# Kernel tuning notes

Hardware: AMD Instinct MI355X
Metric: run time of the kernel (lower is better)

The kernel has to match this reference:

```python
import jax, jax.numpy as jnp
import numpy as np

MAX_STEPS = 128  # upper bound on ACT halting steps (forces halt at last step)
EPS = 0.01


def setup_inputs() -> dict:
    key = jax.random.key(0)
    ks = jax.random.split(key, 8)
    IN, H, OUT = 4096, 4096, 4096
    def lin(k, fan_in, shape):
        return jax.random.normal(k, shape, jnp.float32) / np.float32(np.sqrt(fan_in))
    return {
        "x": jax.random.normal(ks[0], (IN,), jnp.float32),
        "s": jax.random.normal(ks[1], (H,), jnp.float32),
        "W_hidden": lin(ks[2], 1 + IN + H, (H, 1 + IN + H)),
        "b_hidden": lin(ks[3], 1 + IN + H, (H,)),
        "W_halt": lin(ks[4], H, (1, H)),
        "b_halt": lin(ks[5], H, (1,)),
        "W_out": lin(ks[6], H, (OUT, H)),
        "b_out": lin(ks[7], H, (OUT,)),
    }


def _act_forward(x, s, W_hidden, b_hidden, W_halt, b_halt, W_out, b_out):
    OUT = W_out.shape[0]

    def step(carry, i):
        state, cum, acc_out, acc_state, done, ponder = carry
        # flag = 1 on the first step (x1), 0 afterwards (x0)
        flag = jnp.where(i == 0, 1.0, 0.0).astype(x.dtype)
        z = jnp.concatenate([flag[None], x, state])          # [1+IN+H]
        new_state = W_hidden @ z + b_hidden                  # [H]
        p = jax.nn.sigmoid(W_halt @ new_state + b_halt)[0]   # scalar halt prob
        will_halt = (cum + p >= 1.0 - EPS) | (i == MAX_STEPS - 1)
        active = jnp.logical_not(done)
        # last step's weight is the remainder 1 - sum(previous p)
        w = jnp.where(active, jnp.where(will_halt, 1.0 - cum, p), 0.0)
        acc_out = acc_out + w * (W_out @ new_state + b_out)
        acc_state = acc_state + w * new_state
        ponder = jnp.where(active & will_halt,
                           i.astype(x.dtype) + 1.0 + (1.0 - cum), ponder)
        state = jnp.where(active, new_state, state)
        cum = jnp.where(active, cum + p, cum)
        done = done | will_halt
        return (state, cum, acc_out, acc_state, done, ponder), None

    init = (s,
            jnp.zeros((), x.dtype),
            jnp.zeros((OUT,), x.dtype),
            jnp.zeros_like(s),
            jnp.zeros((), jnp.bool_),
            jnp.zeros((), x.dtype))
    (state, cum, out, hid, done, ponder), _ = jax.lax.scan(
        step, init, jnp.arange(MAX_STEPS))
    return out, hid, ponder[None]


def reference(x, s, W_hidden, b_hidden, W_halt, b_halt, W_out, b_out):
    return _act_forward(x, s, W_hidden, b_hidden, W_halt, b_halt, W_out, b_out)
```

## Files before the change

### kernel.cpp

```cpp
#include <hip/hip_runtime.h>
#include <hip/hip_cooperative_groups.h>

namespace cg = cooperative_groups;

#define K_PRE 6

#define O_CUM    0
#define O_DONE   128
#define O_WSUM   256
#define O_PONDER 257
#define O_AXB    512
#define O_P0     4608
#define O_Q0     12800
#define O_ACCH   20992
#define O_NS0    25088
#define O_NS1    29184

__device__ __forceinline__ int zi(int c) { return c + (c >> 5); }

__global__ __launch_bounds__(1024) void k_step(
    int i,
    const float* __restrict__ x, const float* __restrict__ s,
    const float* __restrict__ Wh, const float* __restrict__ bh,
    const float* __restrict__ Whalt, const float* __restrict__ bhalt,
    float* __restrict__ wsb)
{
    const int tid  = threadIdx.x;
    const int lane = tid & 63;
    const int wid  = tid >> 6;
    const int q    = blockIdx.x >> 8;
    const int row  = ((blockIdx.x & 255) << 4) + wid;

    __shared__ float zb[4225];
    __shared__ float red[16];

    const int pre = (4 - ((row + 1) & 3)) & 3;
    float* pbW = wsb + ((i & 1) ? O_Q0 : O_P0);

    if (i == 0) {
        const float* src = q ? s : x;
        for (int k = tid; k < 4096; k += 1024) zb[zi(k)] = src[k];
        __syncthreads();

        const float* WhR = Wh + (size_t)row * 8193;
        const int start  = q ? 4097 : 1;
        const int n4     = (4096 - pre) >> 2;
        const float4* W4 = reinterpret_cast<const float4*>(WhR + start + pre);
        float a0=0.f, a1=0.f, a2=0.f, a3=0.f;
        if (lane < pre) a0 = WhR[start + lane] * zb[zi(lane)];
        #pragma unroll 8
        for (int j = lane; j < n4; j += 64) {
            float4 wv = W4[j];
            int c = pre + 4 * j;
            a0 += wv.x * zb[zi(c)];
            a1 += wv.y * zb[zi(c + 1)];
            a2 += wv.z * zb[zi(c + 2)];
            a3 += wv.w * zb[zi(c + 3)];
        }
        for (int c = pre + 4 * n4 + lane; c < 4096; c += 64)
            a0 += WhR[start + c] * zb[zi(c)];
        float acc = (a0 + a1) + (a2 + a3);
        #pragma unroll
        for (int off = 32; off; off >>= 1) acc += __shfl_xor(acc, off, 64);
        if (lane == 0) {
            if (q == 0) {
                wsb[O_AXB + row] = acc + bh[row];
                pbW[row]         = acc + WhR[0];
            } else {
                pbW[4096 + row]  = acc;
            }
        }
        return;
    }

    const float doneB = (i >= 2) ? wsb[O_DONE + i - 2] : 0.0f;
    if (doneB != 0.0f) {
        if (blockIdx.x == 0 && tid == 0) {
            wsb[O_CUM + i - 1]  = wsb[O_CUM + i - 2];
            wsb[O_DONE + i - 1] = 1.0f;
        }
        return;
    }
    const float cumB = (i >= 2) ? wsb[O_CUM + i - 2] : 0.0f;

    const float* pbR  = wsb + (((i - 1) & 1) ? O_Q0 : O_P0);
    const float* bias = (i == 1) ? bh : (wsb + O_AXB);
    float4 u0 = reinterpret_cast<const float4*>(pbR)[tid];
    float4 u1 = reinterpret_cast<const float4*>(pbR + 4096)[tid];
    float4 bb = reinterpret_cast<const float4*>(bias)[tid];
    float4 hw = reinterpret_cast<const float4*>(Whalt)[tid];
    float4 nsv;
    nsv.x = u0.x + u1.x + bb.x;  nsv.y = u0.y + u1.y + bb.y;
    nsv.z = u0.z + u1.z + bb.z;  nsv.w = u0.w + u1.w + bb.w;
    if ((tid >> 9) == q) {
        int lc = 4 * tid - 2048 * q;
        zb[zi(lc)]   = nsv.x; zb[zi(lc+1)] = nsv.y;
        zb[zi(lc+2)] = nsv.z; zb[zi(lc+3)] = nsv.w;
    }
    float part = hw.x*nsv.x + hw.y*nsv.y + hw.z*nsv.z + hw.w*nsv.w;
    #pragma unroll
    for (int off = 32; off; off >>= 1) part += __shfl_xor(part, off, 64);
    if (lane == 0) red[wid] = part;
    __syncthreads();
    float logit = bhalt[0];
    #pragma unroll
    for (int j = 0; j < 16; ++j) logit += red[j];
    const float p         = 1.0f / (1.0f + expf(-logit));
    const bool  will_halt = (cumB + p >= 0.99f) || ((i - 1) == 127);
    const float w         = will_halt ? (1.0f - cumB) : p;

    if (blockIdx.x == 0 && tid == 0) {
        wsb[O_CUM + i - 1]  = cumB + p;
        wsb[O_DONE + i - 1] = will_halt ? 1.0f : 0.0f;
        if (i == 1) wsb[O_WSUM] = w; else wsb[O_WSUM] += w;
        if (will_halt) wsb[O_PONDER] = (float)(i - 1) + 1.0f + (1.0f - cumB);
    }
    if (blockIdx.x == 0) {
        float4* aH = reinterpret_cast<float4*>(wsb + O_ACCH);
        if (i == 1) {
            float4 t; t.x = w*nsv.x; t.y = w*nsv.y; t.z = w*nsv.z; t.w = w*nsv.w;
            aH[tid] = t;
        } else {
            float4 t = aH[tid];
            t.x += w*nsv.x; t.y += w*nsv.y; t.z += w*nsv.z; t.w += w*nsv.w;
            aH[tid] = t;
        }
    }
    if (i == K_PRE && blockIdx.x == 1)
        reinterpret_cast<float4*>(wsb + (((i - 1) & 1) ? O_NS1 : O_NS0))[tid] = nsv;

    if (i < K_PRE && !will_halt) {
        const float* WhR = Wh + (size_t)row * 8193;
        const int start  = 4097 + 2048 * q;
        const int n4     = (2048 - pre) >> 2;
        const float4* W4 = reinterpret_cast<const float4*>(WhR + start + pre);
        float a0=0.f, a1=0.f, a2=0.f, a3=0.f;
        if (lane < pre) a0 = WhR[start + lane] * zb[zi(lane)];
        #pragma unroll 8
        for (int j = lane; j < n4; j += 64) {
            float4 wv = W4[j];
            int c = pre + 4 * j;
            a0 += wv.x * zb[zi(c)];
            a1 += wv.y * zb[zi(c + 1)];
            a2 += wv.z * zb[zi(c + 2)];
            a3 += wv.w * zb[zi(c + 3)];
        }
        for (int c = pre + 4 * n4 + lane; c < 2048; c += 64)
            a0 += WhR[start + c] * zb[zi(c)];
        float acc = (a0 + a1) + (a2 + a3);
        #pragma unroll
        for (int off = 32; off; off >>= 1) acc += __shfl_xor(acc, off, 64);
        if (lane == 0) pbW[(q << 12) + row] = acc;
    }
}

__global__ __launch_bounds__(1024, 4) void k_tail(
    const float* __restrict__ x, const float* __restrict__ Wh,
    const float* __restrict__ bh, const float* __restrict__ Whalt,
    const float* __restrict__ bhalt, float* __restrict__ wsb)
{
    cg::grid_group grid = cg::this_grid();
    if (wsb[O_DONE + K_PRE - 1] != 0.0f) return;

    const int tid  = threadIdx.x;
    const int lane = tid & 63;
    const int wid  = tid >> 6;
    const int gw   = blockIdx.x * 16 + wid;

    float* ns0 = wsb + O_NS0;
    float* ns1 = wsb + O_NS1;

    __shared__ float xl[4096];
    __shared__ float red[16];
    for (int k = tid; k < 4096; k += 1024) xl[k] = x[k];
    __syncthreads();

    const float* WhR   = Wh + (size_t)gw * 8193;
    const float4* wh4  = reinterpret_cast<const float4*>(Whalt);
    const float bh_r   = bh[gw];
    const float bhalt0 = bhalt[0];

    float cum = wsb[O_CUM + K_PRE - 1];
    float wsuml = 0.f, ponder = 0.f;

    for (int i = K_PRE; i < 128; ++i) {
        const float* st = (i & 1) ? ns0 : ns1;
        float*      nsc = (i & 1) ? ns1 : ns0;

        float acc = 0.0f;
        #pragma unroll 8
        for (int k = lane; k < 4096; k += 64) acc += WhR[1 + k] * xl[k];
        #pragma unroll 8
        for (int k = lane; k < 4096; k += 64) acc += WhR[4097 + k] * st[k];
        #pragma unroll
        for (int off = 32; off; off >>= 1) acc += __shfl_xor(acc, off, 64);
        if (lane == 0) nsc[gw] = acc + bh_r;
        grid.sync();

        const float4* ns4 = reinterpret_cast<const float4*>(nsc);
        float4 nv = ns4[tid], hw = wh4[tid];
        float part = hw.x*nv.x + hw.y*nv.y + hw.z*nv.z + hw.w*nv.w;
        #pragma unroll
        for (int off = 32; off; off >>= 1) part += __shfl_xor(part, off, 64);
        if (lane == 0) red[wid] = part;
        __syncthreads();
        float logit = bhalt0;
        #pragma unroll
        for (int j = 0; j < 16; ++j) logit += red[j];
        const float p         = 1.0f / (1.0f + expf(-logit));
        const bool  will_halt = (cum + p >= 0.99f) || (i == 127);
        const float w         = will_halt ? (1.0f - cum) : p;

        if (blockIdx.x == 0) {
            float4* aH = reinterpret_cast<float4*>(wsb + O_ACCH);
            float4 t = aH[tid];
            t.x += w*nv.x; t.y += w*nv.y; t.z += w*nv.z; t.w += w*nv.w;
            aH[tid] = t;
        }
        wsuml += w;

        if (will_halt) { ponder = (float)i + 1.0f + (1.0f - cum); break; }
        cum += p;
        grid.sync();
    }

    if (blockIdx.x == 0 && tid == 0) {
        wsb[O_WSUM]  += wsuml;
        wsb[O_PONDER] = ponder;
    }
}

__global__ __launch_bounds__(1024) void k_out(
    const float* __restrict__ Wo, const float* __restrict__ bo,
    const float* __restrict__ wsb, float* __restrict__ out)
{
    const int tid  = threadIdx.x;
    const int lane = tid & 63;
    const int wid  = tid >> 6;
    const int row  = blockIdx.x * 16 + wid;

    __shared__ float zb[4225];
    for (int k = tid; k < 4096; k += 1024) zb[zi(k)] = wsb[O_ACCH + k];
    __syncthreads();

    const float4* Wo4 = reinterpret_cast<const float4*>(Wo + (size_t)row * 4096);
    float b0=0.f, b1=0.f, b2=0.f, b3=0.f;
    #pragma unroll 8
    for (int j = lane; j < 1024; j += 64) {
        float4 wv = Wo4[j];
        int c = 4 * j;
        b0 += wv.x * zb[zi(c)];
        b1 += wv.y * zb[zi(c + 1)];
        b2 += wv.z * zb[zi(c + 2)];
        b3 += wv.w * zb[zi(c + 3)];
    }
    float acc = (b0 + b1) + (b2 + b3);
    #pragma unroll
    for (int off = 32; off; off >>= 1) acc += __shfl_xor(acc, off, 64);
    if (lane == 0) out[row] = acc + wsb[O_WSUM] * bo[row];

    const int gtid = blockIdx.x * 1024 + tid;
    if (gtid < 4096) out[4096 + gtid] = wsb[O_ACCH + gtid];
    if (gtid == 0)   out[8192] = wsb[O_PONDER];
}

extern "C" void kernel_launch(void* const* d_in, const int* in_sizes, int n_in,
                              void* d_out, int out_size, void* d_ws, size_t ws_size,
                              hipStream_t stream) {
    const float* x     = (const float*)d_in[0];
    const float* s     = (const float*)d_in[1];
    const float* Wh    = (const float*)d_in[2];
    const float* bh    = (const float*)d_in[3];
    const float* Whalt = (const float*)d_in[4];
    const float* bhalt = (const float*)d_in[5];
    const float* Wo    = (const float*)d_in[6];
    const float* bo    = (const float*)d_in[7];
    float* out = (float*)d_out;
    float* wsb = (float*)d_ws;

    for (int i = 0; i <= K_PRE; ++i)
        k_step<<<512, 1024, 0, stream>>>(i, x, s, Wh, bh, Whalt, bhalt, wsb);

    {
        void* args[] = { (void*)&x, (void*)&Wh, (void*)&bh, (void*)&Whalt,
                         (void*)&bhalt, (void*)&wsb };
        hipLaunchCooperativeKernel((void*)k_tail, dim3(256), dim3(1024),
                                   args, 0, stream);
    }
    k_out<<<256, 1024, 0, stream>>>(Wo, bo, wsb, out);
}
```

Before: 193.2 us.

## Stage weight rows into LDS via async global_load_lds and halve k_step grid

```diff
diff --git a/kernel.cpp b/kernel.cpp
--- a/kernel.cpp
+++ b/kernel.cpp
@@ -18,6 +18,21 @@
 
 __device__ __forceinline__ int zi(int c) { return c + (c >> 5); }
 
+__device__ __forceinline__ void stage512(const float4* __restrict__ g, int nf4,
+                                         float4* wb, int lane) {
+    #pragma unroll
+    for (int k = 0; k < 8; ++k) {
+        int jj = (k << 6) + lane;
+        if (jj >= nf4) jj = nf4 - 1;
+        __builtin_amdgcn_global_load_lds(
+            (const __attribute__((address_space(1))) void*)(g + jj),
+            (__attribute__((address_space(3))) void*)(wb + (k << 6)), 16, 0, 0);
+    }
+}
+
+#define WAIT_VM0   asm volatile("s_waitcnt vmcnt(0)" ::: "memory")
+#define WAIT_LGKM0 asm volatile("s_waitcnt lgkmcnt(0)" ::: "memory")
+
 __global__ __launch_bounds__(1024) void k_step(
     int i,
     const float* __restrict__ x, const float* __restrict__ s,
@@ -28,47 +43,84 @@
     const int tid  = threadIdx.x;
     const int lane = tid & 63;
     const int wid  = tid >> 6;
-    const int q    = blockIdx.x >> 8;
-    const int row  = ((blockIdx.x & 255) << 4) + wid;
-
-    __shared__ float zb[4225];
-    __shared__ float red[16];
+    const int row  = blockIdx.x * 16 + wid;
+
+    __shared__ float  zb[4225];
+    __shared__ float  red[16];
+    __shared__ float4 wbuf[16][512];
+    float4* wb = wbuf[wid];
 
     const int pre = (4 - ((row + 1) & 3)) & 3;
     float* pbW = wsb + ((i & 1) ? O_Q0 : O_P0);
+    const float* WhR = Wh + (size_t)row * 8193;
 
     if (i == 0) {
-        const float* src = q ? s : x;
-        for (int k = tid; k < 4096; k += 1024) zb[zi(k)] = src[k];
+        for (int k = tid; k < 4096; k += 1024) zb[zi(k)] = x[k];
         __syncthreads();
-
-        const float* WhR = Wh + (size_t)row * 8193;
-        const int start  = q ? 4097 : 1;
-        const int n4     = (4096 - pre) >> 2;
-        const float4* W4 = reinterpret_cast<const float4*>(WhR + start + pre);
-        float a0=0.f, a1=0.f, a2=0.f, a3=0.f;
-        if (lane < pre) a0 = WhR[start + lane] * zb[zi(lane)];
-        #pragma unroll 8
-        for (int j = lane; j < n4; j += 64) {
-            float4 wv = W4[j];
-            int c = pre + 4 * j;
-            a0 += wv.x * zb[zi(c)];
-            a1 += wv.y * zb[zi(c + 1)];
-            a2 += wv.z * zb[zi(c + 2)];
-            a3 += wv.w * zb[zi(c + 3)];
-        }
-        for (int c = pre + 4 * n4 + lane; c < 4096; c += 64)
-            a0 += WhR[start + c] * zb[zi(c)];
-        float acc = (a0 + a1) + (a2 + a3);
-        #pragma unroll
-        for (int off = 32; off; off >>= 1) acc += __shfl_xor(acc, off, 64);
-        if (lane == 0) {
-            if (q == 0) {
+        {
+            const int start = 1, cs = start + pre, n4h = (4096 - pre) >> 2;
+            const float4* g = reinterpret_cast<const float4*>(WhR + cs);
+            stage512(g, 512, wb, lane);
+            float a0=0.f, a1=0.f, a2=0.f, a3=0.f;
+            if (lane < pre) a0 = WhR[start + lane] * zb[zi(lane)];
+            WAIT_VM0;
+            #pragma unroll 8
+            for (int j = lane; j < 512; j += 64) {
+                float4 wv = wb[j]; int c = pre + 4 * j;
+                a0 += wv.x * zb[zi(c)];   a1 += wv.y * zb[zi(c + 1)];
+                a2 += wv.z * zb[zi(c + 2)]; a3 += wv.w * zb[zi(c + 3)];
+            }
+            WAIT_LGKM0;
+            stage512(g + 512, n4h - 512, wb, lane);
+            WAIT_VM0;
+            #pragma unroll 8
+            for (int j = 512 + lane; j < n4h; j += 64) {
+                float4 wv = wb[j - 512]; int c = pre + 4 * j;
+                a0 += wv.x * zb[zi(c)];   a1 += wv.y * zb[zi(c + 1)];
+                a2 += wv.z * zb[zi(c + 2)]; a3 += wv.w * zb[zi(c + 3)];
+            }
+            for (int c = pre + 4 * n4h + lane; c < 4096; c += 64)
+                a0 += WhR[start + c] * zb[zi(c)];
+            float acc = (a0 + a1) + (a2 + a3);
+            #pragma unroll
+            for (int off = 32; off; off >>= 1) acc += __shfl_xor(acc, off, 64);
+            if (lane == 0) {
                 wsb[O_AXB + row] = acc + bh[row];
                 pbW[row]         = acc + WhR[0];
-            } else {
-                pbW[4096 + row]  = acc;
-            }
+            }
+        }
+        __syncthreads();
+        for (int k = tid; k < 4096; k += 1024) zb[zi(k)] = s[k];
+        __syncthreads();
+        {
+            const int start = 4097, cs = start + pre, n4h = (4096 - pre) >> 2;
+            const float4* g = reinterpret_cast<const float4*>(WhR + cs);
+            WAIT_LGKM0;
+            stage512(g, 512, wb, lane);
+            float a0=0.f, a1=0.f, a2=0.f, a3=0.f;
+            if (lane < pre) a0 = WhR[start + lane] * zb[zi(lane)];
+            WAIT_VM0;
+            #pragma unroll 8
+            for (int j = lane; j < 512; j += 64) {
+                float4 wv = wb[j]; int c = pre + 4 * j;
+                a0 += wv.x * zb[zi(c)];   a1 += wv.y * zb[zi(c + 1)];
+                a2 += wv.z * zb[zi(c + 2)]; a3 += wv.w * zb[zi(c + 3)];
+            }
+            WAIT_LGKM0;
+            stage512(g + 512, n4h - 512, wb, lane);
+            WAIT_VM0;
+            #pragma unroll 8
+            for (int j = 512 + lane; j < n4h; j += 64) {
+                float4 wv = wb[j - 512]; int c = pre + 4 * j;
+                a0 += wv.x * zb[zi(c)];   a1 += wv.y * zb[zi(c + 1)];
+                a2 += wv.z * zb[zi(c + 2)]; a3 += wv.w * zb[zi(c + 3)];
+            }
+            for (int c = pre + 4 * n4h + lane; c < 4096; c += 64)
+                a0 += WhR[start + c] * zb[zi(c)];
+            float acc = (a0 + a1) + (a2 + a3);
+            #pragma unroll
+            for (int off = 32; off; off >>= 1) acc += __shfl_xor(acc, off, 64);
+            if (lane == 0) pbW[4096 + row] = acc;
         }
         return;
     }
@@ -92,11 +144,9 @@
     float4 nsv;
     nsv.x = u0.x + u1.x + bb.x;  nsv.y = u0.y + u1.y + bb.y;
     nsv.z = u0.z + u1.z + bb.z;  nsv.w = u0.w + u1.w + bb.w;
-    if ((tid >> 9) == q) {
-        int lc = 4 * tid - 2048 * q;
-        zb[zi(lc)]   = nsv.x; zb[zi(lc+1)] = nsv.y;
-        zb[zi(lc+2)] = nsv.z; zb[zi(lc+3)] = nsv.w;
-    }
+    { int c = 4 * tid;
+      zb[zi(c)]   = nsv.x; zb[zi(c+1)] = nsv.y;
+      zb[zi(c+2)] = nsv.z; zb[zi(c+3)] = nsv.w; }
     float part = hw.x*nsv.x + hw.y*nsv.y + hw.z*nsv.z + hw.w*nsv.w;
     #pragma unroll
     for (int off = 32; off; off >>= 1) part += __shfl_xor(part, off, 64);
@@ -130,27 +180,31 @@
         reinterpret_cast<float4*>(wsb + (((i - 1) & 1) ? O_NS1 : O_NS0))[tid] = nsv;
 
     if (i < K_PRE && !will_halt) {
-        const float* WhR = Wh + (size_t)row * 8193;
-        const int start  = 4097 + 2048 * q;
-        const int n4     = (2048 - pre) >> 2;
-        const float4* W4 = reinterpret_cast<const float4*>(WhR + start + pre);
-        float a0=0.f, a1=0.f, a2=0.f, a3=0.f;
-        if (lane < pre) a0 = WhR[start + lane] * zb[zi(lane)];
-        #pragma unroll 8
-        for (int j = lane; j < n4; j += 64) {
-            float4 wv = W4[j];
-            int c = pre + 4 * j;
-            a0 += wv.x * zb[zi(c)];
-            a1 += wv.y * zb[zi(c + 1)];
-            a2 += wv.z * zb[zi(c + 2)];
-            a3 += wv.w * zb[zi(c + 3)];
-        }
-        for (int c = pre + 4 * n4 + lane; c < 2048; c += 64)
-            a0 += WhR[start + c] * zb[zi(c)];
-        float acc = (a0 + a1) + (a2 + a3);
         #pragma unroll
-        for (int off = 32; off; off >>= 1) acc += __shfl_xor(acc, off, 64);
-        if (lane == 0) pbW[(q << 12) + row] = acc;
+        for (int q = 0; q < 2; ++q) {
+            const int startq = 4097 + 2048 * q;
+            const int csq    = startq + pre;
+            const int n4q    = (2048 - pre) >> 2;
+            const int zo     = 2048 * q;
+            const float4* gq = reinterpret_cast<const float4*>(WhR + csq);
+            WAIT_LGKM0;
+            stage512(gq, n4q, wb, lane);
+            float a0=0.f, a1=0.f, a2=0.f, a3=0.f;
+            if (lane < pre) a0 = WhR[startq + lane] * zb[zi(zo + lane)];
+            WAIT_VM0;
+            #pragma unroll 8
+            for (int j = lane; j < n4q; j += 64) {
+                float4 wv = wb[j]; int c = zo + pre + 4 * j;
+                a0 += wv.x * zb[zi(c)];   a1 += wv.y * zb[zi(c + 1)];
+                a2 += wv.z * zb[zi(c + 2)]; a3 += wv.w * zb[zi(c + 3)];
+            }
+            for (int c2 = pre + 4 * n4q + lane; c2 < 2048; c2 += 64)
+                a0 += WhR[startq + c2] * zb[zi(zo + c2)];
+            float acc = (a0 + a1) + (a2 + a3);
+            #pragma unroll
+            for (int off = 32; off; off >>= 1) acc += __shfl_xor(acc, off, 64);
+            if (lane == 0) pbW[(q << 12) + row] = acc;
+        }
     }
 }
 
@@ -239,20 +293,31 @@
     const int wid  = tid >> 6;
     const int row  = blockIdx.x * 16 + wid;
 
-    __shared__ float zb[4225];
+    __shared__ float  zb[4225];
+    __shared__ float4 wbuf[16][512];
+    float4* wb = wbuf[wid];
+
     for (int k = tid; k < 4096; k += 1024) zb[zi(k)] = wsb[O_ACCH + k];
     __syncthreads();
 
-    const float4* Wo4 = reinterpret_cast<const float4*>(Wo + (size_t)row * 4096);
+    const float4* WoR4 = reinterpret_cast<const float4*>(Wo + (size_t)row * 4096);
+    stage512(WoR4, 512, wb, lane);
     float b0=0.f, b1=0.f, b2=0.f, b3=0.f;
+    WAIT_VM0;
     #pragma unroll 8
-    for (int j = lane; j < 1024; j += 64) {
-        float4 wv = Wo4[j];
-        int c = 4 * j;
-        b0 += wv.x * zb[zi(c)];
-        b1 += wv.y * zb[zi(c + 1)];
-        b2 += wv.z * zb[zi(c + 2)];
-        b3 += wv.w * zb[zi(c + 3)];
+    for (int j = lane; j < 512; j += 64) {
+        float4 wv = wb[j]; int c = 4 * j;
+        b0 += wv.x * zb[zi(c)];   b1 += wv.y * zb[zi(c + 1)];
+        b2 += wv.z * zb[zi(c + 2)]; b3 += wv.w * zb[zi(c + 3)];
+    }
+    WAIT_LGKM0;
+    stage512(WoR4 + 512, 512, wb, lane);
+    WAIT_VM0;
+    #pragma unroll 8
+    for (int j = 512 + lane; j < 1024; j += 64) {
+        float4 wv = wb[j - 512]; int c = 4 * j;
+        b0 += wv.x * zb[zi(c)];   b1 += wv.y * zb[zi(c + 1)];
+        b2 += wv.z * zb[zi(c + 2)]; b3 += wv.w * zb[zi(c + 3)];
     }
     float acc = (b0 + b1) + (b2 + b3);
     #pragma unroll
@@ -279,7 +344,7 @@
     float* wsb = (float*)d_ws;
 
     for (int i = 0; i <= K_PRE; ++i)
-        k_step<<<512, 1024, 0, stream>>>(i, x, s, Wh, bh, Whalt, bhalt, wsb);
+        k_step<<<256, 1024, 0, stream>>>(i, x, s, Wh, bh, Whalt, bhalt, wsb);
 
     {
         void* args[] = { (void*)&x, (void*)&Wh, (void*)&bh, (void*)&Whalt,
```

New measurement: 193.7 us. Within noise of the previous version (+0.2%).

## Restructure GEMV kernels to block-wide rows with batched float4 loads

Applied to the files above, without the earlier changes.

```diff
diff --git a/kernel.cpp b/kernel.cpp
--- a/kernel.cpp
+++ b/kernel.cpp
@@ -4,6 +4,8 @@
 namespace cg = cooperative_groups;
 
 #define K_PRE 6
+#define NB 256
+#define NT 1024
 
 #define O_CUM    0
 #define O_DONE   128
@@ -18,7 +20,7 @@
 
 __device__ __forceinline__ int zi(int c) { return c + (c >> 5); }
 
-__global__ __launch_bounds__(1024) void k_step(
+__global__ __launch_bounds__(NT) void k_step(
     int i,
     const float* __restrict__ x, const float* __restrict__ s,
     const float* __restrict__ Wh, const float* __restrict__ bh,
@@ -28,47 +30,72 @@
     const int tid  = threadIdx.x;
     const int lane = tid & 63;
     const int wid  = tid >> 6;
-    const int q    = blockIdx.x >> 8;
-    const int row  = ((blockIdx.x & 255) << 4) + wid;
-
-    __shared__ float zb[4225];
-    __shared__ float red[16];
-
-    const int pre = (4 - ((row + 1) & 3)) & 3;
+
+    __shared__ float zb1[4225];
+    __shared__ float zb2[4225];
+    __shared__ float redH[16];
+    __shared__ float redR[16][16];
+
     float* pbW = wsb + ((i & 1) ? O_Q0 : O_P0);
 
     if (i == 0) {
-        const float* src = q ? s : x;
-        for (int k = tid; k < 4096; k += 1024) zb[zi(k)] = src[k];
+        for (int k = tid; k < 4096; k += NT) { zb1[zi(k)] = x[k]; zb2[zi(k)] = s[k]; }
         __syncthreads();
-
-        const float* WhR = Wh + (size_t)row * 8193;
-        const int start  = q ? 4097 : 1;
-        const int n4     = (4096 - pre) >> 2;
-        const float4* W4 = reinterpret_cast<const float4*>(WhR + start + pre);
-        float a0=0.f, a1=0.f, a2=0.f, a3=0.f;
-        if (lane < pre) a0 = WhR[start + lane] * zb[zi(lane)];
-        #pragma unroll 8
-        for (int j = lane; j < n4; j += 64) {
-            float4 wv = W4[j];
-            int c = pre + 4 * j;
-            a0 += wv.x * zb[zi(c)];
-            a1 += wv.y * zb[zi(c + 1)];
-            a2 += wv.z * zb[zi(c + 2)];
-            a3 += wv.w * zb[zi(c + 3)];
-        }
-        for (int c = pre + 4 * n4 + lane; c < 4096; c += 64)
-            a0 += WhR[start + c] * zb[zi(c)];
-        float acc = (a0 + a1) + (a2 + a3);
-        #pragma unroll
-        for (int off = 32; off; off >>= 1) acc += __shfl_xor(acc, off, 64);
-        if (lane == 0) {
-            if (q == 0) {
-                wsb[O_AXB + row] = acc + bh[row];
-                pbW[row]         = acc + WhR[0];
-            } else {
-                pbW[4096 + row]  = acc;
-            }
+        for (int g = 0; g < 4; ++g) {
+            float4 wx[4], wsv[4];
+            float  px[4], ps[4];
+            int    pres[4], n4s[4];
+            #pragma unroll
+            for (int rr = 0; rr < 4; ++rr) {
+                const int row = blockIdx.x * 16 + g * 4 + rr;
+                const int pre = (4 - ((row + 1) & 3)) & 3;
+                const int n4  = (4096 - pre) >> 2;
+                pres[rr] = pre; n4s[rr] = n4;
+                const float* base = Wh + (size_t)row * 8193;
+                if (tid < n4) {
+                    wx[rr]  = *(const float4*)(base + 1    + pre + 4 * tid);
+                    wsv[rr] = *(const float4*)(base + 4097 + pre + 4 * tid);
+                }
+            }
+            #pragma unroll
+            for (int rr = 0; rr < 4; ++rr) {
+                float ax = 0.f, as = 0.f;
+                const int pre = pres[rr], n4 = n4s[rr];
+                if (tid < n4) {
+                    const int u = pre + 4 * tid;
+                    ax = wx[rr].x*zb1[zi(u)]   + wx[rr].y*zb1[zi(u+1)]
+                       + wx[rr].z*zb1[zi(u+2)] + wx[rr].w*zb1[zi(u+3)];
+                    as = wsv[rr].x*zb2[zi(u)]   + wsv[rr].y*zb2[zi(u+1)]
+                       + wsv[rr].z*zb2[zi(u+2)] + wsv[rr].w*zb2[zi(u+3)];
+                }
+                if (tid == 1008 + rr) {
+                    const float* base = Wh + (size_t)(blockIdx.x*16 + g*4 + rr) * 8193;
+                    for (int u = 0; u < pre; ++u)
+                        { ax += base[1+u]*zb1[zi(u)]; as += base[4097+u]*zb2[zi(u)]; }
+                    for (int u = pre + 4*n4; u < 4096; ++u)
+                        { ax += base[1+u]*zb1[zi(u)]; as += base[4097+u]*zb2[zi(u)]; }
+                }
+                px[rr] = ax; ps[rr] = as;
+            }
+            #pragma unroll
+            for (int rr = 0; rr < 4; ++rr) {
+                #pragma unroll
+                for (int off = 32; off; off >>= 1) {
+                    px[rr] += __shfl_xor(px[rr], off, 64);
+                    ps[rr] += __shfl_xor(ps[rr], off, 64);
+                }
+                if (lane == 0) { redR[rr][wid] = px[rr]; redR[8 + rr][wid] = ps[rr]; }
+            }
+            __syncthreads();
+            if (tid < 4) {
+                float xd = 0.f, sd = 0.f;
+                #pragma unroll
+                for (int j2 = 0; j2 < 16; ++j2) { xd += redR[tid][j2]; sd += redR[8+tid][j2]; }
+                const int row = blockIdx.x * 16 + g * 4 + tid;
+                wsb[O_AXB + row] = xd + bh[row];
+                pbW[row] = (xd + sd) + Wh[(size_t)row * 8193];
+            }
+            __syncthreads();
         }
         return;
     }
@@ -85,26 +112,23 @@
 
     const float* pbR  = wsb + (((i - 1) & 1) ? O_Q0 : O_P0);
     const float* bias = (i == 1) ? bh : (wsb + O_AXB);
-    float4 u0 = reinterpret_cast<const float4*>(pbR)[tid];
-    float4 u1 = reinterpret_cast<const float4*>(pbR + 4096)[tid];
-    float4 bb = reinterpret_cast<const float4*>(bias)[tid];
-    float4 hw = reinterpret_cast<const float4*>(Whalt)[tid];
+    float4 u0 = ((const float4*)pbR)[tid];
+    float4 bb = ((const float4*)bias)[tid];
+    float4 hw = ((const float4*)Whalt)[tid];
     float4 nsv;
-    nsv.x = u0.x + u1.x + bb.x;  nsv.y = u0.y + u1.y + bb.y;
-    nsv.z = u0.z + u1.z + bb.z;  nsv.w = u0.w + u1.w + bb.w;
-    if ((tid >> 9) == q) {
-        int lc = 4 * tid - 2048 * q;
-        zb[zi(lc)]   = nsv.x; zb[zi(lc+1)] = nsv.y;
-        zb[zi(lc+2)] = nsv.z; zb[zi(lc+3)] = nsv.w;
-    }
+    nsv.x = u0.x + bb.x;  nsv.y = u0.y + bb.y;
+    nsv.z = u0.z + bb.z;  nsv.w = u0.w + bb.w;
+    { int c = 4 * tid;
+      zb1[zi(c)]   = nsv.x; zb1[zi(c+1)] = nsv.y;
+      zb1[zi(c+2)] = nsv.z; zb1[zi(c+3)] = nsv.w; }
     float part = hw.x*nsv.x + hw.y*nsv.y + hw.z*nsv.z + hw.w*nsv.w;
     #pragma unroll
     for (int off = 32; off; off >>= 1) part += __shfl_xor(part, off, 64);
-    if (lane == 0) red[wid] = part;
+    if (lane == 0) redH[wid] = part;
     __syncthreads();
     float logit = bhalt[0];
     #pragma unroll
-    for (int j = 0; j < 16; ++j) logit += red[j];
+    for (int j = 0; j < 16; ++j) logit += redH[j];
     const float p         = 1.0f / (1.0f + expf(-logit));
     const bool  will_halt = (cumB + p >= 0.99f) || ((i - 1) == 127);
     const float w         = will_halt ? (1.0f - cumB) : p;
@@ -130,31 +154,54 @@
         reinterpret_cast<float4*>(wsb + (((i - 1) & 1) ? O_NS1 : O_NS0))[tid] = nsv;
 
     if (i < K_PRE && !will_halt) {
-        const float* WhR = Wh + (size_t)row * 8193;
-        const int start  = 4097 + 2048 * q;
-        const int n4     = (2048 - pre) >> 2;
-        const float4* W4 = reinterpret_cast<const float4*>(WhR + start + pre);
-        float a0=0.f, a1=0.f, a2=0.f, a3=0.f;
-        if (lane < pre) a0 = WhR[start + lane] * zb[zi(lane)];
-        #pragma unroll 8
-        for (int j = lane; j < n4; j += 64) {
-            float4 wv = W4[j];
-            int c = pre + 4 * j;
-            a0 += wv.x * zb[zi(c)];
-            a1 += wv.y * zb[zi(c + 1)];
-            a2 += wv.z * zb[zi(c + 2)];
-            a3 += wv.w * zb[zi(c + 3)];
-        }
-        for (int c = pre + 4 * n4 + lane; c < 2048; c += 64)
-            a0 += WhR[start + c] * zb[zi(c)];
-        float acc = (a0 + a1) + (a2 + a3);
-        #pragma unroll
-        for (int off = 32; off; off >>= 1) acc += __shfl_xor(acc, off, 64);
-        if (lane == 0) pbW[(q << 12) + row] = acc;
+        for (int g = 0; g < 2; ++g) {
+            float4 wv[8];
+            float  prt[8];
+            int    pres[8], n4s[8];
+            #pragma unroll
+            for (int rr = 0; rr < 8; ++rr) {
+                const int row = blockIdx.x * 16 + g * 8 + rr;
+                const int pre = (4 - ((row + 1) & 3)) & 3;
+                const int n4  = (4096 - pre) >> 2;
+                pres[rr] = pre; n4s[rr] = n4;
+                if (tid < n4)
+                    wv[rr] = *(const float4*)(Wh + (size_t)row * 8193 + 4097 + pre + 4 * tid);
+            }
+            #pragma unroll
+            for (int rr = 0; rr < 8; ++rr) {
+                float a = 0.f;
+                const int pre = pres[rr], n4 = n4s[rr];
+                if (tid < n4) {
+                    const int u = pre + 4 * tid;
+                    a = wv[rr].x*zb1[zi(u)]   + wv[rr].y*zb1[zi(u+1)]
+                      + wv[rr].z*zb1[zi(u+2)] + wv[rr].w*zb1[zi(u+3)];
+                }
+                if (tid == 1016 + rr) {
+                    const float* base = Wh + (size_t)(blockIdx.x*16 + g*8 + rr) * 8193 + 4097;
+                    for (int u = 0; u < pre; ++u)            a += base[u] * zb1[zi(u)];
+                    for (int u = pre + 4*n4; u < 4096; ++u)  a += base[u] * zb1[zi(u)];
+                }
+                prt[rr] = a;
+            }
+            #pragma unroll
+            for (int rr = 0; rr < 8; ++rr) {
+                #pragma unroll
+                for (int off = 32; off; off >>= 1) prt[rr] += __shfl_xor(prt[rr], off, 64);
+                if (lane == 0) redR[rr][wid] = prt[rr];
+            }
+            __syncthreads();
+            if (tid < 8) {
+                float d = 0.f;
+                #pragma unroll
+                for (int j2 = 0; j2 < 16; ++j2) d += redR[tid][j2];
+                pbW[blockIdx.x * 16 + g * 8 + tid] = d;
+            }
+            if (g == 0) __syncthreads();
+        }
     }
 }
 
-__global__ __launch_bounds__(1024, 4) void k_tail(
+__global__ __launch_bounds__(NT, 4) void k_tail(
     const float* __restrict__ x, const float* __restrict__ Wh,
     const float* __restrict__ bh, const float* __restrict__ Whalt,
     const float* __restrict__ bhalt, float* __restrict__ wsb)
@@ -172,7 +219,7 @@
 
     __shared__ float xl[4096];
     __shared__ float red[16];
-    for (int k = tid; k < 4096; k += 1024) xl[k] = x[k];
+    for (int k = tid; k < 4096; k += NT) xl[k] = x[k];
     __syncthreads();
 
     const float* WhR   = Wh + (size_t)gw * 8193;
@@ -230,36 +277,52 @@
     }
 }
 
-__global__ __launch_bounds__(1024) void k_out(
+__global__ __launch_bounds__(NT) void k_out(
     const float* __restrict__ Wo, const float* __restrict__ bo,
     const float* __restrict__ wsb, float* __restrict__ out)
 {
     const int tid  = threadIdx.x;
     const int lane = tid & 63;
     const int wid  = tid >> 6;
-    const int row  = blockIdx.x * 16 + wid;
-
-    __shared__ float zb[4225];
-    for (int k = tid; k < 4096; k += 1024) zb[zi(k)] = wsb[O_ACCH + k];
+
+    __shared__ float zb1[4225];
+    __shared__ float redR[16][16];
+    for (int k = tid; k < 4096; k += NT) zb1[zi(k)] = wsb[O_ACCH + k];
     __syncthreads();
 
-    const float4* Wo4 = reinterpret_cast<const float4*>(Wo + (size_t)row * 4096);
-    float b0=0.f, b1=0.f, b2=0.f, b3=0.f;
-    #pragma unroll 8
-    for (int j = lane; j < 1024; j += 64) {
-        float4 wv = Wo4[j];
-        int c = 4 * j;
-        b0 += wv.x * zb[zi(c)];
-        b1 += wv.y * zb[zi(c + 1)];
-        b2 += wv.z * zb[zi(c + 2)];
-        b3 += wv.w * zb[zi(c + 3)];
-    }
-    float acc = (b0 + b1) + (b2 + b3);
-    #pragma unroll
-    for (int off = 32; off; off >>= 1) acc += __shfl_xor(acc, off, 64);
-    if (lane == 0) out[row] = acc + wsb[O_WSUM] * bo[row];
-
-    const int gtid = blockIdx.x * 1024 + tid;
+    const float wsum = wsb[O_WSUM];
+    for (int g = 0; g < 2; ++g) {
+        float4 wv[8];
+        float  prt[8];
+        #pragma unroll
+        for (int rr = 0; rr < 8; ++rr) {
+            const int row = blockIdx.x * 16 + g * 8 + rr;
+            wv[rr] = ((const float4*)(Wo + (size_t)row * 4096))[tid];
+        }
+        #pragma unroll
+        for (int rr = 0; rr < 8; ++rr) {
+            const int u = 4 * tid;
+            prt[rr] = wv[rr].x*zb1[zi(u)]   + wv[rr].y*zb1[zi(u+1)]
+                    + wv[rr].z*zb1[zi(u+2)] + wv[rr].w*zb1[zi(u+3)];
+        }
+        #pragma unroll
+        for (int rr = 0; rr < 8; ++rr) {
+            #pragma unroll
+            for (int off = 32; off; off >>= 1) prt[rr] += __shfl_xor(prt[rr], off, 64);
+            if (lane == 0) redR[rr][wid] = prt[rr];
+        }
+        __syncthreads();
+        if (tid < 8) {
+            float d = 0.f;
+            #pragma unroll
+            for (int j2 = 0; j2 < 16; ++j2) d += redR[tid][j2];
+            const int row = blockIdx.x * 16 + g * 8 + tid;
+            out[row] = d + wsum * bo[row];
+        }
+        if (g == 0) __syncthreads();
+    }
+
+    const int gtid = blockIdx.x * NT + tid;
     if (gtid < 4096) out[4096 + gtid] = wsb[O_ACCH + gtid];
     if (gtid == 0)   out[8192] = wsb[O_PONDER];
 }
@@ -279,13 +342,13 @@
     float* wsb = (float*)d_ws;
 
     for (int i = 0; i <= K_PRE; ++i)
-        k_step<<<512, 1024, 0, stream>>>(i, x, s, Wh, bh, Whalt, bhalt, wsb);
+        k_step<<<NB, NT, 0, stream>>>(i, x, s, Wh, bh, Whalt, bhalt, wsb);
 
     {
         void* args[] = { (void*)&x, (void*)&Wh, (void*)&bh, (void*)&Whalt,
                          (void*)&bhalt, (void*)&wsb };
-        hipLaunchCooperativeKernel((void*)k_tail, dim3(256), dim3(1024),
+        hipLaunchCooperativeKernel((void*)k_tail, dim3(256), dim3(NT),
                                    args, 0, stream);
     }
-    k_out<<<256, 1024, 0, stream>>>(Wo, bo, wsb, out);
+    k_out<<<NB, NT, 0, stream>>>(Wo, bo, wsb, out);
 }
```

Measured after the change: 216.8 us (median of 3 runs). +12.2%, slower.
